# Performance work log

Measured on AMD Instinct MI355X. Metric: run time of the kernel, lower is better.

The kernel has to match this reference:

```python
import jax, jax.numpy as jnp
import numpy as np

WS = 8            # window size (square)
N = WS * WS       # tokens per window = 64
DIM = 192
HEADS = 6
HDIM = DIM // HEADS
SCALE = HDIM ** -0.5


def _rel_pos_index(ws=WS):
    coords = np.stack(np.meshgrid(np.arange(ws), np.arange(ws), indexing='ij'))  # [2,ws,ws]
    cf = coords.reshape(2, -1)                       # [2, N]
    rc = (cf[:, :, None] - cf[:, None, :]).transpose(1, 2, 0).astype(np.int64)  # [N,N,2]
    rc[:, :, 0] += ws - 1
    rc[:, :, 1] += ws - 1
    rc[:, :, 0] *= 2 * ws - 1
    return jnp.asarray(rc.sum(-1))                   # [N, N]

REL_IDX = _rel_pos_index()


def _linear(x, w, b=None):
    y = jnp.einsum('...i,oi->...o', x, w)
    return y if b is None else y + b


def _diff_attn(q_t, k_t, v_t, q_r, k_r, v_r, bias, lam):
    # q,k,v: [B, H, N, d]; bias: [H, N, N]; lam scalar
    at = jax.nn.softmax(jnp.einsum('bhqd,bhkd->bhqk', q_t * SCALE, k_t) + bias, axis=-1)
    ar = jax.nn.softmax(jnp.einsum('bhqd,bhkd->bhqk', q_r * SCALE, k_r) + bias, axis=-1)
    dt = at - lam * ar
    dr = ar - lam * at
    ot = jnp.einsum('bhqk,bhkd->bhqd', dt, v_t)
    orf = jnp.einsum('bhqk,bhkd->bhqd', dr, v_r)
    return ot, orf


def _heads(x, B):
    # [B, N, C] -> [B, H, N, d]
    return x.reshape(B, N, HEADS, HDIM).transpose(0, 2, 1, 3)


def _unheads(x, B):
    return x.transpose(0, 2, 1, 3).reshape(B, N, DIM)


def setup_inputs() -> dict:
    key = jax.random.key(0)
    ks = jax.random.split(key, 16)
    nW = 1024
    p = lambda k, shp: (jax.random.normal(k, shp, jnp.float32) * 0.02)
    return {
        'x_windows': jax.random.normal(ks[0], (nW, N, DIM), jnp.float32),
        'y_windows': jax.random.normal(ks[1], (nW, N, DIM), jnp.float32),
        'sa_qkv_w': p(ks[2], (3 * DIM, DIM)), 'sa_qkv_b': jnp.zeros((3 * DIM,), jnp.float32),
        'sa_ct_w': p(ks[3], (DIM, DIM)), 'sa_cr_w': p(ks[4], (DIM, DIM)),
        'ca_q_w': p(ks[5], (DIM, DIM)), 'ca_q_b': jnp.zeros((DIM,), jnp.float32),
        'ca_kv_w': p(ks[6], (2 * DIM, DIM)), 'ca_kv_b': jnp.zeros((2 * DIM,), jnp.float32),
        'ca_ct_w': p(ks[7], (DIM, DIM)), 'ca_cr_w': p(ks[8], (DIM, DIM)),
        'rpb_table': p(ks[9], ((2 * WS - 1) * (2 * WS - 1), HEADS)),
        'proj_sa_w': p(ks[10], (DIM, DIM)), 'proj_sa_b': jnp.zeros((DIM,), jnp.float32),
        'proj_ca_w': p(ks[11], (DIM, DIM)), 'proj_ca_b': jnp.zeros((DIM,), jnp.float32),
        'lambda_sa': jnp.float32(0.1), 'lambda_ca': jnp.float32(0.1),
        'sa_enh': jnp.float32(0.1), 'ca_enh': jnp.float32(0.1),
    }


def reference(x_windows, y_windows, sa_qkv_w, sa_qkv_b, sa_ct_w, sa_cr_w,
              ca_q_w, ca_q_b, ca_kv_w, ca_kv_b, ca_ct_w, ca_cr_w,
              rpb_table, proj_sa_w, proj_sa_b, proj_ca_w, proj_ca_b,
              lambda_sa, lambda_ca, sa_enh, ca_enh):
    B = x_windows.shape[0]
    bias = rpb_table[REL_IDX.reshape(-1)].reshape(N, N, HEADS).transpose(2, 0, 1)  # [H,N,N]

    # ---- Self-attention branch (batch-dim concat) ----
    t_enh = x_windows + sa_enh * _linear(y_windows, sa_cr_w)
    r_enh = y_windows + sa_enh * _linear(x_windows, sa_ct_w)
    qkv_t = _linear(t_enh, sa_qkv_w, sa_qkv_b).reshape(B, N, 3, HEADS, HDIM).transpose(2, 0, 3, 1, 4)
    qkv_r = _linear(r_enh, sa_qkv_w, sa_qkv_b).reshape(B, N, 3, HEADS, HDIM).transpose(2, 0, 3, 1, 4)
    lam_sa = jnp.clip(jax.nn.sigmoid(lambda_sa), 0.01, 0.99)
    ot, orf = _diff_attn(qkv_t[0], qkv_t[1], qkv_t[2], qkv_r[0], qkv_r[1], qkv_r[2], bias, lam_sa)
    sa_t = _linear(_unheads(ot, B), proj_sa_w, proj_sa_b)
    sa_r = _linear(_unheads(orf, B), proj_sa_w, proj_sa_b)
    sa_out = jnp.concatenate([sa_t, sa_r], axis=0)  # [2B, N, C]

    # ---- Cross-attention branch (seq-dim concat) ----
    t_enh = x_windows + ca_enh * _linear(y_windows, ca_cr_w)
    r_enh = y_windows + ca_enh * _linear(x_windows, ca_ct_w)
    q_t = _heads(_linear(t_enh, ca_q_w, ca_q_b), B)
    q_r = _heads(_linear(r_enh, ca_q_w, ca_q_b), B)
    xcat = jnp.concatenate([t_enh, r_enh], axis=1)  # [B, 2N, C]
    kv = _linear(xcat, ca_kv_w, ca_kv_b).reshape(B, 2 * N, 2, HEADS, HDIM).transpose(2, 0, 3, 1, 4)
    k, v = kv[0], kv[1]
    k_t, k_r = k[:, :, :N], k[:, :, N:]
    v_t, v_r = v[:, :, :N], v[:, :, N:]
    lam_ca = jnp.clip(jax.nn.sigmoid(lambda_ca), 0.01, 0.99)
    ot, orf = _diff_attn(q_t, k_t, v_t, q_r, k_r, v_r, bias, lam_ca)
    ca_t = _linear(_unheads(ot, B), proj_ca_w, proj_ca_b)
    ca_r = _linear(_unheads(orf, B), proj_ca_w, proj_ca_b)
    ca_out = jnp.concatenate([ca_t, ca_r], axis=1)  # [B, 2N, C]

    # pack into a single array: [4B, N, C]
    return jnp.concatenate([sa_out, ca_out.reshape(2 * B, N, DIM)], axis=0)
```

## Files before the change

### kernel.cpp

```cpp
#include <hip/hip_runtime.h>

#define KD 192
#define H6 6

typedef __attribute__((ext_vector_type(8))) short bf16x8;
typedef __attribute__((ext_vector_type(4))) float f32x4;

__device__ __forceinline__ unsigned short f2bf(float f) {
  unsigned u = __float_as_uint(f);
  u += 0x7FFFu + ((u >> 16) & 1u);
  return (unsigned short)(u >> 16);
}

__global__ void bias_k(const float* __restrict__ tab, float* __restrict__ biasw) {
  int t = blockIdx.x * 256 + threadIdx.x;
  if (t >= H6 * 64 * 64) return;
  int h = t >> 12, rem = t & 4095, i = rem >> 6, j = rem & 63;
  int idx = ((i >> 3) - (j >> 3) + 7) * 15 + ((i & 7) - (j & 7) + 7);
  biasw[t] = tab[idx * H6 + h];
}

__global__ void convert_k(
    const float* __restrict__ sa_qkv_w, const float* __restrict__ sa_ct_w,
    const float* __restrict__ sa_cr_w, const float* __restrict__ ca_q_w,
    const float* __restrict__ ca_kv_w, const float* __restrict__ ca_ct_w,
    const float* __restrict__ ca_cr_w, const float* __restrict__ proj_sa_w,
    const float* __restrict__ proj_ca_w,
    const float* __restrict__ ca_q_b, const float* __restrict__ ca_kv_b,
    unsigned short* __restrict__ wqkv, unsigned short* __restrict__ wct_sa,
    unsigned short* __restrict__ wcr_sa, unsigned short* __restrict__ wca,
    unsigned short* __restrict__ wct_ca, unsigned short* __restrict__ wcr_ca,
    unsigned short* __restrict__ wpsa, unsigned short* __restrict__ wpca,
    float* __restrict__ bca)
{
  int t = blockIdx.x * 256 + threadIdx.x;
  if (t < 110592) {
    int i = t << 2;
    const float* s; unsigned short* d;
    if (i < 110592)      { s = sa_qkv_w + i;            d = wqkv + i; }
    else if (i < 147456) { s = sa_ct_w + (i - 110592);  d = wct_sa + (i - 110592); }
    else if (i < 184320) { s = sa_cr_w + (i - 147456);  d = wcr_sa + (i - 147456); }
    else if (i < 221184) { s = ca_q_w + (i - 184320);   d = wca + (i - 184320); }
    else if (i < 294912) { s = ca_kv_w + (i - 221184);  d = wca + 36864 + (i - 221184); }
    else if (i < 331776) { s = ca_ct_w + (i - 294912);  d = wct_ca + (i - 294912); }
    else if (i < 368640) { s = ca_cr_w + (i - 331776);  d = wcr_ca + (i - 331776); }
    else if (i < 405504) { s = proj_sa_w + (i - 368640); d = wpsa + (i - 368640); }
    else                 { s = proj_ca_w + (i - 405504); d = wpca + (i - 405504); }
    float4 v = *(const float4*)s;
    ushort4 p;
    p.x = f2bf(v.x); p.y = f2bf(v.y); p.z = f2bf(v.z); p.w = f2bf(v.w);
    *(ushort4*)d = p;
  } else if (t < 110592 + 144) {
    int i = (t - 110592) << 2;
    const float* s = (i < 192) ? (ca_q_b + i) : (ca_kv_b + (i - 192));
    *(float4*)(bca + i) = *(const float4*)s;
  }
}

struct FQArgs {
  const unsigned short* Wc[4];
  const unsigned short* Wq[4];
  const float* bias[4];
  unsigned short* dq[4];
  unsigned short* dk[4];
  unsigned short* dv[4];
};

__global__ __launch_bounds__(256) void fqkv_k(
    const float* __restrict__ x, const float* __restrict__ y,
    const float* __restrict__ sap, const float* __restrict__ cap,
    FQArgs args, float SC)
{
  __shared__ short Al[64][200], Wl[64][200], El[64][200];
  const int tid = threadIdx.x;
  const int mblk = blockIdx.x, z = blockIdx.y;
  const int row = tid >> 2, cb = (tid & 3) * 48;
  const float* A    = (z & 1) ? x : y;
  const float* resd = (z & 1) ? y : x;
  const float sc = (z < 2) ? *sap : *cap;

  {
    const float* ap = A + ((long)mblk * 64 + row) * KD + cb;
#pragma unroll
    for (int j = 0; j < 12; ++j) {
      float4 v = *(const float4*)(ap + 4 * j);
      ushort4 p;
      p.x = f2bf(v.x); p.y = f2bf(v.y); p.z = f2bf(v.z); p.w = f2bf(v.w);
      *(ushort4*)&Al[row][cb + 4 * j] = p;
    }
  }
  const int lane = tid & 63, wv = tid >> 6;
  const int qn = lane & 15, g = lane >> 4;
  const int mloc = 16 * wv + 4 * g;
  const f32x4 zero = {0.f, 0.f, 0.f, 0.f};

  for (int ct = 0; ct < 3; ++ct) {
    {
      const unsigned short* Wp = args.Wc[z] + ((long)ct * 64 + row) * KD + cb;
#pragma unroll
      for (int j = 0; j < 6; ++j)
        *(float4*)&Wl[row][cb + 8 * j] = *(const float4*)(Wp + 8 * j);
    }
    __syncthreads();
    f32x4 acc[4];
#pragma unroll
    for (int nt = 0; nt < 4; ++nt) acc[nt] = zero;
#pragma unroll
    for (int ks = 0; ks < 6; ++ks) {
      bf16x8 a = *(const bf16x8*)&Al[16 * wv + qn][32 * ks + 8 * g];
#pragma unroll
      for (int nt = 0; nt < 4; ++nt) {
        bf16x8 bfr = *(const bf16x8*)&Wl[16 * nt + qn][32 * ks + 8 * g];
        acc[nt] = __builtin_amdgcn_mfma_f32_16x16x32_bf16(a, bfr, acc[nt], 0, 0, 0);
      }
    }
#pragma unroll
    for (int nt = 0; nt < 4; ++nt) {
      const int c = ct * 64 + 16 * nt + qn;
#pragma unroll
      for (int r = 0; r < 4; ++r)
        El[mloc + r][c] =
            f2bf(resd[((long)mblk * 64 + mloc + r) * KD + c] + sc * acc[nt][r]);
    }
    __syncthreads();
  }

  for (int wt = 0; wt < 9; ++wt) {
    {
      const unsigned short* Wp = args.Wq[z] + ((long)wt * 64 + row) * KD + cb;
#pragma unroll
      for (int j = 0; j < 6; ++j)
        *(float4*)&Wl[row][cb + 8 * j] = *(const float4*)(Wp + 8 * j);
    }
    __syncthreads();
    f32x4 acc[4];
#pragma unroll
    for (int nt = 0; nt < 4; ++nt) acc[nt] = zero;
#pragma unroll
    for (int ks = 0; ks < 6; ++ks) {
      bf16x8 a = *(const bf16x8*)&El[16 * wv + qn][32 * ks + 8 * g];
#pragma unroll
      for (int nt = 0; nt < 4; ++nt) {
        bf16x8 bfr = *(const bf16x8*)&Wl[16 * nt + qn][32 * ks + 8 * g];
        acc[nt] = __builtin_amdgcn_mfma_f32_16x16x32_bf16(a, bfr, acc[nt], 0, 0, 0);
      }
    }
#pragma unroll
    for (int nt = 0; nt < 4; ++nt) {
      const int cg = wt * 64 + 16 * nt + qn;
      const int idx = (cg >= 384) ? 2 : ((cg >= 192) ? 1 : 0);
      const int cc = cg - idx * KD;
      const int h = cc >> 5, d = cc & 31;
      const float bv = args.bias[z][cg];
      const float sca = (idx == 0) ? SC : 1.f;
      const long bwh = (long)mblk * H6 + h;
      if (idx < 2) {
        unsigned short* dst = idx ? args.dk[z] : args.dq[z];
#pragma unroll
        for (int r = 0; r < 4; ++r)
          dst[(bwh * 64 + (mloc + r)) * 32 + d] = f2bf((acc[nt][r] + bv) * sca);
      } else {
        ushort4 p;
        p.x = f2bf(acc[nt][0] + bv);
        p.y = f2bf(acc[nt][1] + bv);
        p.z = f2bf(acc[nt][2] + bv);
        p.w = f2bf(acc[nt][3] + bv);
        *(ushort4*)&args.dv[z][(bwh * 32 + d) * 64 + mloc] = p;
      }
    }
    __syncthreads();
  }
}

__device__ __forceinline__ void softmax_rows2(f32x4 (&S)[4][2]) {
#pragma unroll
  for (int nt = 0; nt < 2; ++nt) {
    float mx = -3.0e38f;
#pragma unroll
    for (int mt = 0; mt < 4; ++mt)
#pragma unroll
      for (int r = 0; r < 4; ++r) mx = fmaxf(mx, S[mt][nt][r]);
    mx = fmaxf(mx, __shfl_xor(mx, 16));
    mx = fmaxf(mx, __shfl_xor(mx, 32));
    float sm = 0.f;
#pragma unroll
    for (int mt = 0; mt < 4; ++mt)
#pragma unroll
      for (int r = 0; r < 4; ++r) {
        float p = __expf(S[mt][nt][r] - mx);
        S[mt][nt][r] = p;
        sm += p;
      }
    sm += __shfl_xor(sm, 16);
    sm += __shfl_xor(sm, 32);
    const float inv = 1.f / sm;
#pragma unroll
    for (int mt = 0; mt < 4; ++mt)
#pragma unroll
      for (int r = 0; r < 4; ++r) S[mt][nt][r] *= inv;
  }
}

struct FAArgs {
  const unsigned short* q[2];
  const unsigned short* k[2];
  const unsigned short* vT[2];
  const float* lamp[2];
  const unsigned short* w[2];
  const float* pb[2];
  float* ot[2];
  float* orr[2];
  long ostride[2];
};

__global__ __launch_bounds__(768, 3) void fattn_k(
    FAArgs args, const float* __restrict__ biasw, long pstride)
{
  __shared__ short Ol[2][64][200];
  __shared__ short Pl[12][32][72];
  const int tid = threadIdx.x;
  const int wv = tid >> 6, lane = tid & 63;
  const int qn = lane & 15, g = lane >> 4;
  const int b = blockIdx.x, z = blockIdx.y;
  const int h = wv >> 1, qoff = (wv & 1) * 32;
  const long base = ((long)b * H6 + h) * 2048;
  const unsigned short* qb = args.q[z];
  const unsigned short* kb = args.k[z];
  const unsigned short* vTb = args.vT[z];
  float lam = 1.f / (1.f + __expf(-*args.lamp[z]));
  lam = fminf(fmaxf(lam, 0.01f), 0.99f);
  const float* bh = biasw + (long)h * 4096;
  short (*pl)[72] = Pl[wv];
  const f32x4 zero = {0.f, 0.f, 0.f, 0.f};

  f32x4 st[4][2], sr[4][2];
#pragma unroll
  for (int mt = 0; mt < 4; ++mt)
#pragma unroll
    for (int nt = 0; nt < 2; ++nt) {
      f32x4 bv = *(const f32x4*)&bh[(qoff + 16 * nt + qn) * 64 + 16 * mt + 4 * g];
      st[mt][nt] = bv;
      sr[mt][nt] = bv;
    }
  {
    bf16x8 ka[4], qv[2];
#pragma unroll
    for (int mt = 0; mt < 4; ++mt)
      ka[mt] = *(const bf16x8*)&kb[base + (16 * mt + qn) * 32 + 8 * g];
#pragma unroll
    for (int nt = 0; nt < 2; ++nt)
      qv[nt] = *(const bf16x8*)&qb[base + (qoff + 16 * nt + qn) * 32 + 8 * g];
#pragma unroll
    for (int mt = 0; mt < 4; ++mt)
#pragma unroll
      for (int nt = 0; nt < 2; ++nt)
        st[mt][nt] = __builtin_amdgcn_mfma_f32_16x16x32_bf16(ka[mt], qv[nt], st[mt][nt], 0, 0, 0);
#pragma unroll
    for (int mt = 0; mt < 4; ++mt)
      ka[mt] = *(const bf16x8*)&kb[pstride + base + (16 * mt + qn) * 32 + 8 * g];
#pragma unroll
    for (int nt = 0; nt < 2; ++nt)
      qv[nt] = *(const bf16x8*)&qb[pstride + base + (qoff + 16 * nt + qn) * 32 + 8 * g];
#pragma unroll
    for (int mt = 0; mt < 4; ++mt)
#pragma unroll
      for (int nt = 0; nt < 2; ++nt)
        sr[mt][nt] = __builtin_amdgcn_mfma_f32_16x16x32_bf16(ka[mt], qv[nt], sr[mt][nt], 0, 0, 0);
  }
  softmax_rows2(st);
  softmax_rows2(sr);
#pragma unroll
  for (int mt = 0; mt < 4; ++mt)
#pragma unroll
    for (int nt = 0; nt < 2; ++nt)
#pragma unroll
      for (int r = 0; r < 4; ++r) {
        float a = st[mt][nt][r], rr = sr[mt][nt][r];
        st[mt][nt][r] = a - lam * rr;
        sr[mt][nt][r] = rr - lam * a;
      }

#pragma unroll
  for (int p = 0; p < 2; ++p) {
    auto& P = p ? sr : st;
#pragma unroll
    for (int mt = 0; mt < 4; ++mt)
#pragma unroll
      for (int nt = 0; nt < 2; ++nt) {
        ushort4 pk;
        pk.x = f2bf(P[mt][nt][0]); pk.y = f2bf(P[mt][nt][1]);
        pk.z = f2bf(P[mt][nt][2]); pk.w = f2bf(P[mt][nt][3]);
        *(ushort4*)&pl[16 * nt + qn][16 * mt + 4 * g] = pk;
      }
    const unsigned short* vv = p ? (vTb + pstride) : vTb;
    f32x4 oa[2][2];
#pragma unroll
    for (int i = 0; i < 2; ++i)
#pragma unroll
      for (int nt = 0; nt < 2; ++nt) oa[i][nt] = zero;
#pragma unroll
    for (int ks = 0; ks < 2; ++ks) {
      bf16x8 va0 = *(const bf16x8*)&vv[base + (0 + qn) * 64 + 32 * ks + 8 * g];
      bf16x8 va1 = *(const bf16x8*)&vv[base + (16 + qn) * 64 + 32 * ks + 8 * g];
#pragma unroll
      for (int nt = 0; nt < 2; ++nt) {
        bf16x8 pb8 = *(const bf16x8*)&pl[16 * nt + qn][32 * ks + 8 * g];
        oa[0][nt] = __builtin_amdgcn_mfma_f32_16x16x32_bf16(va0, pb8, oa[0][nt], 0, 0, 0);
        oa[1][nt] = __builtin_amdgcn_mfma_f32_16x16x32_bf16(va1, pb8, oa[1][nt], 0, 0, 0);
      }
    }
#pragma unroll
    for (int d16 = 0; d16 < 2; ++d16)
#pragma unroll
      for (int nt = 0; nt < 2; ++nt) {
        ushort4 pk;
        pk.x = f2bf(oa[d16][nt][0]); pk.y = f2bf(oa[d16][nt][1]);
        pk.z = f2bf(oa[d16][nt][2]); pk.w = f2bf(oa[d16][nt][3]);
        *(ushort4*)&Ol[p][qoff + 16 * nt + qn][h * 32 + 16 * d16 + 4 * g] = pk;
      }
  }

  const int cstrip = wv * 16;
  const unsigned short* wz = args.w[z];
  bf16x8 wf[6];
#pragma unroll
  for (int ks = 0; ks < 6; ++ks)
    wf[ks] = *(const bf16x8*)&wz[(long)(cstrip + qn) * KD + 32 * ks + 8 * g];
  f32x4 biasv = *(const f32x4*)&args.pb[z][cstrip + 4 * g];
  __syncthreads();

#pragma unroll
  for (int p = 0; p < 2; ++p) {
    f32x4 acc[4];
#pragma unroll
    for (int mt = 0; mt < 4; ++mt) acc[mt] = zero;
#pragma unroll
    for (int ks = 0; ks < 6; ++ks)
#pragma unroll
      for (int mt = 0; mt < 4; ++mt) {
        bf16x8 of = *(const bf16x8*)&Ol[p][16 * mt + qn][32 * ks + 8 * g];
        acc[mt] = __builtin_amdgcn_mfma_f32_16x16x32_bf16(wf[ks], of, acc[mt], 0, 0, 0);
      }
    float* fo = (p ? args.orr[z] : args.ot[z]) + (long)b * args.ostride[z];
#pragma unroll
    for (int mt = 0; mt < 4; ++mt) {
      f32x4 res;
#pragma unroll
      for (int r = 0; r < 4; ++r) res[r] = acc[mt][r] + biasv[r];
      *(f32x4*)&fo[(long)(16 * mt + qn) * KD + cstrip + 4 * g] = res;
    }
  }
}

__device__ __forceinline__ void diff_attn32(
    const unsigned short* __restrict__ qb, const unsigned short* __restrict__ kb,
    const unsigned short* __restrict__ vTb, long pstride,
    const float* __restrict__ bh, float lam,
    unsigned short* __restrict__ o_t, unsigned short* __restrict__ o_r,
    long base, int b, int h, int qoff, int qn, int g,
    short (*Pl)[32][72])
{
  f32x4 st[4][2], sr[4][2];
#pragma unroll
  for (int mt = 0; mt < 4; ++mt)
#pragma unroll
    for (int nt = 0; nt < 2; ++nt) {
      f32x4 bv = *(const f32x4*)&bh[(qoff + 16 * nt + qn) * 64 + 16 * mt + 4 * g];
      st[mt][nt] = bv;
      sr[mt][nt] = bv;
    }
  {
    bf16x8 ka[4], qv[2];
#pragma unroll
    for (int mt = 0; mt < 4; ++mt)
      ka[mt] = *(const bf16x8*)&kb[base + (16 * mt + qn) * 32 + 8 * g];
#pragma unroll
    for (int nt = 0; nt < 2; ++nt)
      qv[nt] = *(const bf16x8*)&qb[base + (qoff + 16 * nt + qn) * 32 + 8 * g];
#pragma unroll
    for (int mt = 0; mt < 4; ++mt)
#pragma unroll
      for (int nt = 0; nt < 2; ++nt)
        st[mt][nt] = __builtin_amdgcn_mfma_f32_16x16x32_bf16(ka[mt], qv[nt], st[mt][nt], 0, 0, 0);
#pragma unroll
    for (int mt = 0; mt < 4; ++mt)
      ka[mt] = *(const bf16x8*)&kb[pstride + base + (16 * mt + qn) * 32 + 8 * g];
#pragma unroll
    for (int nt = 0; nt < 2; ++nt)
      qv[nt] = *(const bf16x8*)&qb[pstride + base + (qoff + 16 * nt + qn) * 32 + 8 * g];
#pragma unroll
    for (int mt = 0; mt < 4; ++mt)
#pragma unroll
      for (int nt = 0; nt < 2; ++nt)
        sr[mt][nt] = __builtin_amdgcn_mfma_f32_16x16x32_bf16(ka[mt], qv[nt], sr[mt][nt], 0, 0, 0);
  }
  softmax_rows2(st);
  softmax_rows2(sr);
#pragma unroll
  for (int mt = 0; mt < 4; ++mt)
#pragma unroll
    for (int nt = 0; nt < 2; ++nt) {
      ushort4 pt, pr;
#pragma unroll
      for (int r = 0; r < 4; ++r) {
        float a = st[mt][nt][r], rr = sr[mt][nt][r];
        ((unsigned short*)&pt)[r] = f2bf(a - lam * rr);
        ((unsigned short*)&pr)[r] = f2bf(rr - lam * a);
      }
      *(ushort4*)&Pl[0][16 * nt + qn][16 * mt + 4 * g] = pt;
      *(ushort4*)&Pl[1][16 * nt + qn][16 * mt + 4 * g] = pr;
    }
  const f32x4 zero = {0.f, 0.f, 0.f, 0.f};
#pragma unroll
  for (int p = 0; p < 2; ++p) {
    const unsigned short* vv = p ? (vTb + pstride) : vTb;
    unsigned short* outp = p ? o_r : o_t;
    f32x4 oa[2][2];
#pragma unroll
    for (int i = 0; i < 2; ++i)
#pragma unroll
      for (int nt = 0; nt < 2; ++nt) oa[i][nt] = zero;
#pragma unroll
    for (int ks = 0; ks < 2; ++ks) {
      bf16x8 va0 = *(const bf16x8*)&vv[base + (0 + qn) * 64 + 32 * ks + 8 * g];
      bf16x8 va1 = *(const bf16x8*)&vv[base + (16 + qn) * 64 + 32 * ks + 8 * g];
#pragma unroll
      for (int nt = 0; nt < 2; ++nt) {
        bf16x8 pb = *(const bf16x8*)&Pl[p][16 * nt + qn][32 * ks + 8 * g];
        oa[0][nt] = __builtin_amdgcn_mfma_f32_16x16x32_bf16(va0, pb, oa[0][nt], 0, 0, 0);
        oa[1][nt] = __builtin_amdgcn_mfma_f32_16x16x32_bf16(va1, pb, oa[1][nt], 0, 0, 0);
      }
    }
#pragma unroll
    for (int d16 = 0; d16 < 2; ++d16)
#pragma unroll
      for (int nt = 0; nt < 2; ++nt) {
        const int q = qoff + 16 * nt + qn;
        ushort4 pk;
        pk.x = f2bf(oa[d16][nt][0]); pk.y = f2bf(oa[d16][nt][1]);
        pk.z = f2bf(oa[d16][nt][2]); pk.w = f2bf(oa[d16][nt][3]);
        *(ushort4*)&outp[((long)b * 64 + q) * KD + h * 32 + 16 * d16 + 4 * g] = pk;
      }
  }
}

__global__ __launch_bounds__(256) void attn_k(
    const unsigned short* __restrict__ saq, const unsigned short* __restrict__ sak,
    const unsigned short* __restrict__ savT,
    const unsigned short* __restrict__ caq, const unsigned short* __restrict__ cak,
    const unsigned short* __restrict__ cavT,
    const float* __restrict__ biasw, const float* __restrict__ lsp,
    const float* __restrict__ lcp,
    unsigned short* __restrict__ o0, unsigned short* __restrict__ o1,
    unsigned short* __restrict__ o2, unsigned short* __restrict__ o3,
    long pstride)
{
  __shared__ short Pl[4][2][32][72];
  const int wv = threadIdx.x >> 6, lane = threadIdx.x & 63;
  const int qn = lane & 15, g = lane >> 4;
  const int qoff = (wv & 1) * 32;
  const int wh = blockIdx.x * 2 + (wv >> 1);
  const int b = wh / H6, h = wh - b * H6;
  const float* bh = biasw + (long)h * 4096;
  const long base = (long)wh * 2048;
  float ls = 1.f / (1.f + __expf(-*lsp));
  ls = fminf(fmaxf(ls, 0.01f), 0.99f);
  float lc = 1.f / (1.f + __expf(-*lcp));
  lc = fminf(fmaxf(lc, 0.01f), 0.99f);
  diff_attn32(saq, sak, savT, pstride, bh, ls, o0, o1, base, b, h, qoff, qn, g, Pl[wv]);
  diff_attn32(caq, cak, cavT, pstride, bh, lc, o2, o3, base, b, h, qoff, qn, g, Pl[wv]);
}

struct ProjArgs {
  const unsigned short* A[4];
  const unsigned short* W[4];
  const float* bias[4];
  float* o[4];
  long wstride[4];
};

__global__ __launch_bounds__(256) void proj_k(ProjArgs args)
{
  __shared__ short Al[64][200], Wl[64][200];
  const int tid = threadIdx.x;
  const int mblk = blockIdx.x, z = blockIdx.y;
  const int row = tid >> 2, cb = (tid & 3) * 48;
  {
    const unsigned short* A = args.A[z] + ((long)mblk * 64 + row) * KD + cb;
#pragma unroll
    for (int j = 0; j < 6; ++j)
      *(float4*)&Al[row][cb + 8 * j] = *(const float4*)(A + 8 * j);
  }
  const int lane = tid & 63, wv = tid >> 6;
  const int qn = lane & 15, g = lane >> 4;
  const int mloc = 16 * wv + 4 * g;
  const f32x4 zero = {0.f, 0.f, 0.f, 0.f};
  float* fo = args.o[z] + (long)mblk * args.wstride[z];

  for (int ct = 0; ct < 3; ++ct) {
    {
      const unsigned short* Wp = args.W[z] + ((long)ct * 64 + row) * KD + cb;
#pragma unroll
      for (int j = 0; j < 6; ++j)
        *(float4*)&Wl[row][cb + 8 * j] = *(const float4*)(Wp + 8 * j);
    }
    __syncthreads();
    f32x4 acc[4];
#pragma unroll
    for (int nt = 0; nt < 4; ++nt) acc[nt] = zero;
#pragma unroll
    for (int ks = 0; ks < 6; ++ks) {
      bf16x8 a = *(const bf16x8*)&Al[16 * wv + qn][32 * ks + 8 * g];
#pragma unroll
      for (int nt = 0; nt < 4; ++nt) {
        bf16x8 bfr = *(const bf16x8*)&Wl[16 * nt + qn][32 * ks + 8 * g];
        acc[nt] = __builtin_amdgcn_mfma_f32_16x16x32_bf16(a, bfr, acc[nt], 0, 0, 0);
      }
    }
#pragma unroll
    for (int nt = 0; nt < 4; ++nt) {
      const int c = ct * 64 + 16 * nt + qn;
      const float bv = args.bias[z][c];
#pragma unroll
      for (int r = 0; r < 4; ++r)
        fo[(long)(mloc + r) * KD + c] = acc[nt][r] + bv;
    }
    __syncthreads();
  }
}

extern "C" void kernel_launch(void* const* d_in, const int* in_sizes, int n_in,
                              void* d_out, int out_size, void* d_ws, size_t ws_size,
                              hipStream_t stream)
{
  const float* x         = (const float*)d_in[0];
  const float* y         = (const float*)d_in[1];
  const float* sa_qkv_w  = (const float*)d_in[2];
  const float* sa_qkv_b  = (const float*)d_in[3];
  const float* sa_ct_w   = (const float*)d_in[4];
  const float* sa_cr_w   = (const float*)d_in[5];
  const float* ca_q_w    = (const float*)d_in[6];
  const float* ca_q_b    = (const float*)d_in[7];
  const float* ca_kv_w   = (const float*)d_in[8];
  const float* ca_kv_b   = (const float*)d_in[9];
  const float* ca_ct_w   = (const float*)d_in[10];
  const float* ca_cr_w   = (const float*)d_in[11];
  const float* rpb       = (const float*)d_in[12];
  const float* proj_sa_w = (const float*)d_in[13];
  const float* proj_sa_b = (const float*)d_in[14];
  const float* proj_ca_w = (const float*)d_in[15];
  const float* proj_ca_b = (const float*)d_in[16];
  const float* lam_sa_p  = (const float*)d_in[17];
  const float* lam_ca_p  = (const float*)d_in[18];
  const float* sa_enh_p  = (const float*)d_in[19];
  const float* ca_enh_p  = (const float*)d_in[20];
  float* out = (float*)d_out;

  const int M = in_sizes[0] / KD;
  const int B = M / 64;
  const long pstride = (long)B * H6 * 2048;

  char* ws = (char*)d_ws;
  float* biasw = (float*)ws;
  float* bca = (float*)(ws + 98304);
  unsigned short* wqkv   = (unsigned short*)(ws + 100864);
  unsigned short* wca    = (unsigned short*)(ws + 322048);
  unsigned short* wct_sa = (unsigned short*)(ws + 543232);
  unsigned short* wcr_sa = (unsigned short*)(ws + 616960);
  unsigned short* wct_ca = (unsigned short*)(ws + 690688);
  unsigned short* wcr_ca = (unsigned short*)(ws + 764416);
  unsigned short* wpsa   = (unsigned short*)(ws + 838144);
  unsigned short* wpca   = (unsigned short*)(ws + 911872);

  const size_t TEN = (size_t)pstride * 4;
  const size_t NEED = 1048576 + 6 * TEN;
  const bool fused = (ws_size >= NEED);

  const float SC = 0.17677669529663687f;

  convert_k<<<dim3(433), dim3(256), 0, stream>>>(
      sa_qkv_w, sa_ct_w, sa_cr_w, ca_q_w, ca_kv_w, ca_ct_w, ca_cr_w,
      proj_sa_w, proj_ca_w, ca_q_b, ca_kv_b,
      wqkv, wct_sa, wcr_sa, wca, wct_ca, wcr_ca, wpsa, wpca, bca);
  bias_k<<<dim3(96), dim3(256), 0, stream>>>(rpb, biasw);

  if (fused) {
    long off = 1048576;
    unsigned short* saq  = (unsigned short*)(ws + off); off += TEN;
    unsigned short* sak  = (unsigned short*)(ws + off); off += TEN;
    unsigned short* savT = (unsigned short*)(ws + off); off += TEN;
    unsigned short* caq  = (unsigned short*)(ws + off); off += TEN;
    unsigned short* cak  = (unsigned short*)(ws + off); off += TEN;
    unsigned short* cavT = (unsigned short*)(ws + off);

    FQArgs fa;
    fa.Wc[0] = wcr_sa; fa.Wc[1] = wct_sa; fa.Wc[2] = wcr_ca; fa.Wc[3] = wct_ca;
    fa.Wq[0] = wqkv;   fa.Wq[1] = wqkv;   fa.Wq[2] = wca;    fa.Wq[3] = wca;
    fa.bias[0] = sa_qkv_b; fa.bias[1] = sa_qkv_b; fa.bias[2] = bca; fa.bias[3] = bca;
    fa.dq[0] = saq;  fa.dq[1] = saq + pstride;  fa.dq[2] = caq;  fa.dq[3] = caq + pstride;
    fa.dk[0] = sak;  fa.dk[1] = sak + pstride;  fa.dk[2] = cak;  fa.dk[3] = cak + pstride;
    fa.dv[0] = savT; fa.dv[1] = savT + pstride; fa.dv[2] = cavT; fa.dv[3] = cavT + pstride;
    fqkv_k<<<dim3(B, 4), dim3(256), 0, stream>>>(x, y, sa_enh_p, ca_enh_p, fa, SC);

    FAArgs aa;
    aa.q[0] = saq;  aa.q[1] = caq;
    aa.k[0] = sak;  aa.k[1] = cak;
    aa.vT[0] = savT; aa.vT[1] = cavT;
    aa.lamp[0] = lam_sa_p; aa.lamp[1] = lam_ca_p;
    aa.w[0] = wpsa; aa.w[1] = wpca;
    aa.pb[0] = proj_sa_b; aa.pb[1] = proj_ca_b;
    aa.ot[0]  = out;
    aa.orr[0] = out + (long)B * 12288;
    aa.ot[1]  = out + (long)2 * B * 12288;
    aa.orr[1] = out + (long)2 * B * 12288 + 12288;
    aa.ostride[0] = 12288;
    aa.ostride[1] = 24576;
    fattn_k<<<dim3(B, 2), dim3(768), 0, stream>>>(aa, biasw, pstride);
  } else {
    long off = 1048576;
    unsigned short* ob0 = (unsigned short*)(ws + off); off += (long)M * KD * 2;
    unsigned short* ob1 = (unsigned short*)(ws + off); off += (long)M * KD * 2;
    unsigned short* ob2 = (unsigned short*)(ws + off); off += (long)M * KD * 2;
    unsigned short* ob3 = (unsigned short*)(ws + off); off += (long)M * KD * 2;
    unsigned short* caq  = (unsigned short*)(ws + off); off += TEN;
    unsigned short* cak  = (unsigned short*)(ws + off); off += TEN;
    unsigned short* cavT = (unsigned short*)(ws + off);
    unsigned short* saq  = (unsigned short*)d_out;
    unsigned short* sak  = saq + 2 * pstride;
    unsigned short* savT = sak + 2 * pstride;

    FQArgs fa;
    fa.Wc[0] = wcr_sa; fa.Wc[1] = wct_sa; fa.Wc[2] = wcr_ca; fa.Wc[3] = wct_ca;
    fa.Wq[0] = wqkv;   fa.Wq[1] = wqkv;   fa.Wq[2] = wca;    fa.Wq[3] = wca;
    fa.bias[0] = sa_qkv_b; fa.bias[1] = sa_qkv_b; fa.bias[2] = bca; fa.bias[3] = bca;
    fa.dq[0] = saq;  fa.dq[1] = saq + pstride;  fa.dq[2] = caq;  fa.dq[3] = caq + pstride;
    fa.dk[0] = sak;  fa.dk[1] = sak + pstride;  fa.dk[2] = cak;  fa.dk[3] = cak + pstride;
    fa.dv[0] = savT; fa.dv[1] = savT + pstride; fa.dv[2] = cavT; fa.dv[3] = cavT + pstride;
    fqkv_k<<<dim3(B, 4), dim3(256), 0, stream>>>(x, y, sa_enh_p, ca_enh_p, fa, SC);

    attn_k<<<dim3(B * H6 / 2), dim3(256), 0, stream>>>(saq, sak, savT, caq, cak, cavT,
                                                       biasw, lam_sa_p, lam_ca_p,
                                                       ob0, ob1, ob2, ob3, pstride);

    ProjArgs pa;
    pa.A[0] = ob0; pa.A[1] = ob1; pa.A[2] = ob2; pa.A[3] = ob3;
    pa.W[0] = wpsa; pa.W[1] = wpsa; pa.W[2] = wpca; pa.W[3] = wpca;
    pa.bias[0] = proj_sa_b; pa.bias[1] = proj_sa_b; pa.bias[2] = proj_ca_b; pa.bias[3] = proj_ca_b;
    pa.o[0] = out;                       pa.wstride[0] = 12288;
    pa.o[1] = out + (long)B * 12288;     pa.wstride[1] = 12288;
    pa.o[2] = out + (long)2 * B * 12288; pa.wstride[2] = 24576;
    pa.o[3] = out + (long)2 * B * 12288 + 12288; pa.wstride[3] = 24576;
    proj_k<<<dim3(B, 4), dim3(256), 0, stream>>>(pa);
  }
}
```

Baseline: 636.4 us.

## Register-prefetch weight tiles, cache A fragments in registers, use 2x2 wave tiling

Restructures the fused QKV projection kernel. The next weight tile is now prefetched into registers while the current tile's MFMAs run, and the activation fragments are held in registers instead of being reloaded from LDS. The wave tiling changes from 16x64 to 32x32, and the A and E shared buffers are merged to cut LDS use. The aim is to hide global load latency, reduce LDS traffic and raise occupancy, at the cost of more register pressure.

```diff
diff --git a/kernel.cpp b/kernel.cpp
--- a/kernel.cpp
+++ b/kernel.cpp
@@ -71,7 +71,8 @@
     const float* __restrict__ sap, const float* __restrict__ cap,
     FQArgs args, float SC)
 {
-  __shared__ short Al[64][200], Wl[64][200], El[64][200];
+  __shared__ short AE[64][200];
+  __shared__ short Wl[64][200];
   const int tid = threadIdx.x;
   const int mblk = blockIdx.x, z = blockIdx.y;
   const int row = tid >> 2, cb = (tid & 3) * 48;
@@ -79,96 +80,127 @@
   const float* resd = (z & 1) ? y : x;
   const float sc = (z < 2) ? *sap : *cap;
 
+  float4 wpf[6];
   {
     const float* ap = A + ((long)mblk * 64 + row) * KD + cb;
+    const unsigned short* wp = args.Wc[z] + (long)row * KD + cb;
+#pragma unroll
+    for (int j = 0; j < 6; ++j) wpf[j] = *(const float4*)(wp + 8 * j);
 #pragma unroll
     for (int j = 0; j < 12; ++j) {
       float4 v = *(const float4*)(ap + 4 * j);
       ushort4 p;
       p.x = f2bf(v.x); p.y = f2bf(v.y); p.z = f2bf(v.z); p.w = f2bf(v.w);
-      *(ushort4*)&Al[row][cb + 4 * j] = p;
-    }
-  }
+      *(ushort4*)&AE[row][cb + 4 * j] = p;
+    }
+#pragma unroll
+    for (int j = 0; j < 6; ++j) *(float4*)&Wl[row][cb + 8 * j] = wpf[j];
+  }
+  __syncthreads();
+
   const int lane = tid & 63, wv = tid >> 6;
   const int qn = lane & 15, g = lane >> 4;
-  const int mloc = 16 * wv + 4 * g;
+  const int rbase = (wv & 1) * 32, cbase = (wv >> 1) * 32;
   const f32x4 zero = {0.f, 0.f, 0.f, 0.f};
 
+  bf16x8 af[2][6];
+#pragma unroll
+  for (int im = 0; im < 2; ++im)
+#pragma unroll
+    for (int ks = 0; ks < 6; ++ks)
+      af[im][ks] = *(const bf16x8*)&AE[rbase + 16 * im + qn][32 * ks + 8 * g];
+  __syncthreads();
+
+#pragma unroll
   for (int ct = 0; ct < 3; ++ct) {
     {
-      const unsigned short* Wp = args.Wc[z] + ((long)ct * 64 + row) * KD + cb;
-#pragma unroll
-      for (int j = 0; j < 6; ++j)
-        *(float4*)&Wl[row][cb + 8 * j] = *(const float4*)(Wp + 8 * j);
-    }
+      const unsigned short* ns = (ct < 2) ? (args.Wc[z] + (long)(ct + 1) * 12288)
+                                          : args.Wq[z];
+      const unsigned short* wp = ns + (long)row * KD + cb;
+#pragma unroll
+      for (int j = 0; j < 6; ++j) wpf[j] = *(const float4*)(wp + 8 * j);
+    }
+    f32x4 acc[2][2] = {{zero, zero}, {zero, zero}};
+#pragma unroll
+    for (int ks = 0; ks < 6; ++ks) {
+      bf16x8 wf0 = *(const bf16x8*)&Wl[cbase + qn][32 * ks + 8 * g];
+      bf16x8 wf1 = *(const bf16x8*)&Wl[cbase + 16 + qn][32 * ks + 8 * g];
+      acc[0][0] = __builtin_amdgcn_mfma_f32_16x16x32_bf16(af[0][ks], wf0, acc[0][0], 0, 0, 0);
+      acc[1][0] = __builtin_amdgcn_mfma_f32_16x16x32_bf16(af[1][ks], wf0, acc[1][0], 0, 0, 0);
+      acc[0][1] = __builtin_amdgcn_mfma_f32_16x16x32_bf16(af[0][ks], wf1, acc[0][1], 0, 0, 0);
+      acc[1][1] = __builtin_amdgcn_mfma_f32_16x16x32_bf16(af[1][ks], wf1, acc[1][1], 0, 0, 0);
+    }
+#pragma unroll
+    for (int im = 0; im < 2; ++im)
+#pragma unroll
+      for (int in = 0; in < 2; ++in) {
+        const int c = ct * 64 + cbase + 16 * in + qn;
+        const int rl = rbase + 16 * im + 4 * g;
+#pragma unroll
+        for (int r = 0; r < 4; ++r)
+          AE[rl + r][c] = f2bf(resd[((long)mblk * 64 + rl + r) * KD + c] +
+                               sc * acc[im][in][r]);
+      }
     __syncthreads();
-    f32x4 acc[4];
-#pragma unroll
-    for (int nt = 0; nt < 4; ++nt) acc[nt] = zero;
+#pragma unroll
+    for (int j = 0; j < 6; ++j) *(float4*)&Wl[row][cb + 8 * j] = wpf[j];
+    __syncthreads();
+  }
+
+#pragma unroll
+  for (int im = 0; im < 2; ++im)
+#pragma unroll
+    for (int ks = 0; ks < 6; ++ks)
+      af[im][ks] = *(const bf16x8*)&AE[rbase + 16 * im + qn][32 * ks + 8 * g];
+
+  for (int wt = 0; wt < 9; ++wt) {
+    if (wt < 8) {
+      const unsigned short* wp = args.Wq[z] + (long)(wt + 1) * 12288 + (long)row * KD + cb;
+#pragma unroll
+      for (int j = 0; j < 6; ++j) wpf[j] = *(const float4*)(wp + 8 * j);
+    }
+    f32x4 acc[2][2] = {{zero, zero}, {zero, zero}};
 #pragma unroll
     for (int ks = 0; ks < 6; ++ks) {
-      bf16x8 a = *(const bf16x8*)&Al[16 * wv + qn][32 * ks + 8 * g];
-#pragma unroll
-      for (int nt = 0; nt < 4; ++nt) {
-        bf16x8 bfr = *(const bf16x8*)&Wl[16 * nt + qn][32 * ks + 8 * g];
-        acc[nt] = __builtin_amdgcn_mfma_f32_16x16x32_bf16(a, bfr, acc[nt], 0, 0, 0);
-      }
-    }
-#pragma unroll
-    for (int nt = 0; nt < 4; ++nt) {
-      const int c = ct * 64 + 16 * nt + qn;
-#pragma unroll
-      for (int r = 0; r < 4; ++r)
-        El[mloc + r][c] =
-            f2bf(resd[((long)mblk * 64 + mloc + r) * KD + c] + sc * acc[nt][r]);
-    }
-    __syncthreads();
-  }
-
-  for (int wt = 0; wt < 9; ++wt) {
-    {
-      const unsigned short* Wp = args.Wq[z] + ((long)wt * 64 + row) * KD + cb;
-#pragma unroll
-      for (int j = 0; j < 6; ++j)
-        *(float4*)&Wl[row][cb + 8 * j] = *(const float4*)(Wp + 8 * j);
-    }
-    __syncthreads();
-    f32x4 acc[4];
-#pragma unroll
-    for (int nt = 0; nt < 4; ++nt) acc[nt] = zero;
-#pragma unroll
-    for (int ks = 0; ks < 6; ++ks) {
-      bf16x8 a = *(const bf16x8*)&El[16 * wv + qn][32 * ks + 8 * g];
-#pragma unroll
-      for (int nt = 0; nt < 4; ++nt) {
-        bf16x8 bfr = *(const bf16x8*)&Wl[16 * nt + qn][32 * ks + 8 * g];
-        acc[nt] = __builtin_amdgcn_mfma_f32_16x16x32_bf16(a, bfr, acc[nt], 0, 0, 0);
-      }
-    }
-#pragma unroll
-    for (int nt = 0; nt < 4; ++nt) {
-      const int cg = wt * 64 + 16 * nt + qn;
-      const int idx = (cg >= 384) ? 2 : ((cg >= 192) ? 1 : 0);
-      const int cc = cg - idx * KD;
-      const int h = cc >> 5, d = cc & 31;
-      const float bv = args.bias[z][cg];
-      const float sca = (idx == 0) ? SC : 1.f;
-      const long bwh = (long)mblk * H6 + h;
-      if (idx < 2) {
-        unsigned short* dst = idx ? args.dk[z] : args.dq[z];
-#pragma unroll
-        for (int r = 0; r < 4; ++r)
-          dst[(bwh * 64 + (mloc + r)) * 32 + d] = f2bf((acc[nt][r] + bv) * sca);
-      } else {
-        ushort4 p;
-        p.x = f2bf(acc[nt][0] + bv);
-        p.y = f2bf(acc[nt][1] + bv);
-        p.z = f2bf(acc[nt][2] + bv);
-        p.w = f2bf(acc[nt][3] + bv);
-        *(ushort4*)&args.dv[z][(bwh * 32 + d) * 64 + mloc] = p;
-      }
-    }
-    __syncthreads();
+      bf16x8 wf0 = *(const bf16x8*)&Wl[cbase + qn][32 * ks + 8 * g];
+      bf16x8 wf1 = *(const bf16x8*)&Wl[cbase + 16 + qn][32 * ks + 8 * g];
+      acc[0][0] = __builtin_amdgcn_mfma_f32_16x16x32_bf16(af[0][ks], wf0, acc[0][0], 0, 0, 0);
+      acc[1][0] = __builtin_amdgcn_mfma_f32_16x16x32_bf16(af[1][ks], wf0, acc[1][0], 0, 0, 0);
+      acc[0][1] = __builtin_amdgcn_mfma_f32_16x16x32_bf16(af[0][ks], wf1, acc[0][1], 0, 0, 0);
+      acc[1][1] = __builtin_amdgcn_mfma_f32_16x16x32_bf16(af[1][ks], wf1, acc[1][1], 0, 0, 0);
+    }
+#pragma unroll
+    for (int im = 0; im < 2; ++im)
+#pragma unroll
+      for (int in = 0; in < 2; ++in) {
+        const int cg = wt * 64 + cbase + 16 * in + qn;
+        const int idx = (cg >= 384) ? 2 : ((cg >= 192) ? 1 : 0);
+        const int cc = cg - idx * KD;
+        const int h = cc >> 5, d = cc & 31;
+        const float bv = args.bias[z][cg];
+        const long bwh = (long)mblk * H6 + h;
+        const int rl = rbase + 16 * im + 4 * g;
+        if (idx < 2) {
+          const float sca = idx ? 1.f : SC;
+          unsigned short* dst = idx ? args.dk[z] : args.dq[z];
+#pragma unroll
+          for (int r = 0; r < 4; ++r)
+            dst[(bwh * 64 + rl + r) * 32 + d] = f2bf((acc[im][in][r] + bv) * sca);
+        } else {
+          ushort4 p;
+          p.x = f2bf(acc[im][in][0] + bv);
+          p.y = f2bf(acc[im][in][1] + bv);
+          p.z = f2bf(acc[im][in][2] + bv);
+          p.w = f2bf(acc[im][in][3] + bv);
+          *(ushort4*)&args.dv[z][(bwh * 32 + d) * 64 + rl] = p;
+        }
+      }
+    if (wt < 8) {
+      __syncthreads();
+#pragma unroll
+      for (int j = 0; j < 6; ++j) *(float4*)&Wl[row][cb + 8 * j] = wpf[j];
+      __syncthreads();
+    }
   }
 }
 
```

New measurement: 841.8 us. 32.3% more time.
